# Kernel tuning notes

Measured on AMD Instinct MI355X. Metric: run time of the kernel, lower is better.

## Reference

```python
import jax, jax.numpy as jnp
import numpy as np

# Mamba2 hyperparameters (from init_kwargs + mamba_ssm defaults)
D_MODEL = 1024
D_STATE = 64
D_CONV = 4
EXPAND = 2
HEADDIM = 64                      # mamba_ssm default
D_INNER = EXPAND * D_MODEL        # 2048
NHEADS = D_INNER // HEADDIM       # 32
NGROUPS = 1
CONV_DIM = D_INNER + 2 * NGROUPS * D_STATE      # 2176
D_IN_PROJ = 2 * D_INNER + 2 * NGROUPS * D_STATE + NHEADS  # 4256
BATCH, SEQLEN = 4, 2048


def setup_inputs() -> dict:
    key = jax.random.key(0)
    ks = jax.random.split(key, 8)
    x = jax.random.normal(ks[0], (BATCH, SEQLEN, D_MODEL), dtype=jnp.float32)
    W_in = jax.random.normal(ks[1], (D_MODEL, D_IN_PROJ), dtype=jnp.float32) * 0.02
    conv_w = jax.random.normal(ks[2], (CONV_DIM, D_CONV), dtype=jnp.float32) * 0.2
    conv_b = jnp.zeros((CONV_DIM,), dtype=jnp.float32)
    # dt_bias = inverse-softplus of dt ~ U(1e-3, 0.1), as in mamba_ssm init
    dt = jnp.exp(jax.random.uniform(ks[3], (NHEADS,)) * (np.log(0.1) - np.log(1e-3)) + np.log(1e-3))
    dt_bias = dt + jnp.log(-jnp.expm1(-dt))
    A_log = jnp.log(jax.random.uniform(ks[4], (NHEADS,), minval=1.0, maxval=16.0))
    D = jnp.ones((NHEADS,), dtype=jnp.float32)
    norm_w = jnp.ones((D_INNER,), dtype=jnp.float32)
    W_out = jax.random.normal(ks[5], (D_INNER, D_MODEL), dtype=jnp.float32) * 0.02
    return {"x": x, "W_in": W_in, "conv_w": conv_w, "conv_b": conv_b,
            "dt_bias": dt_bias, "A_log": A_log, "D": D, "norm_w": norm_w, "W_out": W_out}


def _mamba2_forward(x, W_in, conv_w, conv_b, dt_bias, A_log, D, norm_w, W_out):
    Bsz, L, _ = x.shape
    zxbcdt = x @ W_in                                   # [B, L, D_IN_PROJ]
    z = zxbcdt[..., :D_INNER]                           # gate
    xBC = zxbcdt[..., D_INNER:D_INNER + CONV_DIM]
    dt = zxbcdt[..., D_INNER + CONV_DIM:]               # [B, L, H]
    dt = jax.nn.softplus(dt + dt_bias)

    # causal depthwise conv1d over time, kernel width D_CONV
    xp = jnp.pad(xBC, ((0, 0), (D_CONV - 1, 0), (0, 0)))
    xc = sum(xp[:, k:k + L, :] * conv_w[:, k] for k in range(D_CONV))
    xBC = jax.nn.silu(xc + conv_b)

    xh = xBC[..., :D_INNER].reshape(Bsz, L, NHEADS, HEADDIM)   # [B,L,H,P]
    Bm = xBC[..., D_INNER:D_INNER + D_STATE]                   # [B,L,N] (ngroups=1)
    Cm = xBC[..., D_INNER + D_STATE:]                          # [B,L,N]
    A = -jnp.exp(A_log)                                        # [H]

    # selective SSM scan: h_t = h_{t-1}*exp(dt_t*A) + dt_t * x_t (outer) B_t ; y_t = C_t . h_t
    def step(h, inp):
        dt_t, x_t, B_t, C_t = inp                 # [B,H],[B,H,P],[B,N],[B,N]
        dA = jnp.exp(dt_t * A)                    # [B,H]
        h = h * dA[..., None, None] + (dt_t[..., None] * x_t)[..., None] * B_t[:, None, None, :]
        y_t = jnp.einsum('bhpn,bn->bhp', h, C_t)
        return h, y_t

    h0 = jnp.zeros((Bsz, NHEADS, HEADDIM, D_STATE), dtype=x.dtype)
    inputs = (jnp.moveaxis(dt, 1, 0), jnp.moveaxis(xh, 1, 0),
              jnp.moveaxis(Bm, 1, 0), jnp.moveaxis(Cm, 1, 0))
    _, ys = jax.lax.scan(step, h0, inputs)                     # [L,B,H,P]
    y = jnp.moveaxis(ys, 0, 1) + xh * D[None, None, :, None]   # skip term D*x
    y = y.reshape(Bsz, L, D_INNER)

    # gated RMSNorm: norm(y * silu(z)) * weight
    y = y * jax.nn.silu(z)
    y = y * jax.lax.rsqrt(jnp.mean(y * y, axis=-1, keepdims=True) + 1e-5) * norm_w
    return y @ W_out


def reference(x, W_in, conv_w, conv_b, dt_bias, A_log, D, norm_w, W_out):
    return _mamba2_forward(x, W_in, conv_w, conv_b, dt_bias, A_log, D, norm_w, W_out)
```

## Files before the change

kernel.cpp:

```cpp
#include <hip/hip_runtime.h>
#include <hip/hip_bf16.h>

#define B_SZ   4
#define SEQ    2048
#define DM     1024
#define DIN    2048
#define DST    64
#define NH     32
#define HD     64
#define DPROJ  4256
#define NPROJ  4224
#define MROWS  (B_SZ*SEQ)
#define QC     64
#define NC     (SEQ/QC)


typedef __attribute__((ext_vector_type(8))) __bf16 bf16x8;
typedef __attribute__((ext_vector_type(4))) __bf16 bf16x4;
typedef __attribute__((ext_vector_type(4))) float  floatx4;

__device__ __forceinline__ int swz(int row, int col) {
    return row * 64 + ((((col >> 3) ^ (row & 7)) << 3) | (col & 7));
}
__device__ __forceinline__ float bfbits2f(unsigned short u) {
    return __uint_as_float(((unsigned int)u) << 16);
}
__device__ __forceinline__ float silu_f(float v) { return v / (1.f + __expf(-v)); }

__global__ __launch_bounds__(256) void prep_cvt_kernel(const float* __restrict__ x,
                                                       const float* __restrict__ W_in,
                                                       const float* __restrict__ W_out,
                                                       const float* __restrict__ norm_w,
                                                       __bf16* __restrict__ xbf,
                                                       __bf16* __restrict__ WinT,
                                                       __bf16* __restrict__ WoutT,
                                                       float* __restrict__ dtraw) {
    __shared__ float smem[16 * 132 + 4096];
    const int bid = blockIdx.x, tid = threadIdx.x;
    if (bid < 1568) {
        float (*tile)[129] = (float (*)[129])smem;
        const float* src; __bf16* dst; const float* scal; int Ksrc, Csrc, mb, kb;
        if (bid < 1056) {
            mb = bid >> 5; kb = bid & 31;
            src = W_in; dst = WinT; scal = nullptr; Ksrc = DM; Csrc = DPROJ;
        } else {
            int t = bid - 1056; mb = t >> 6; kb = t & 63;
            src = W_out; dst = WoutT; scal = norm_w; Ksrc = DIN; Csrc = DM;
        }
        const int K32 = Ksrc >> 5;
        #pragma unroll
        for (int i = 0; i < 4; i++) {
            int idx = tid + 256 * i;
            int kl = idx >> 5, c4 = idx & 31;
            int n = mb * 128 + c4 * 4;
            float4 v = make_float4(0.f, 0.f, 0.f, 0.f);
            if (n < Csrc) v = *(const float4*)(src + (size_t)(kb * 32 + kl) * Csrc + n);
            if (scal) { float s = scal[kb * 32 + kl]; v.x *= s; v.y *= s; v.z *= s; v.w *= s; }
            tile[kl][c4 * 4 + 0] = v.x; tile[kl][c4 * 4 + 1] = v.y;
            tile[kl][c4 * 4 + 2] = v.z; tile[kl][c4 * 4 + 3] = v.w;
        }
        __syncthreads();
        #pragma unroll
        for (int i = 0; i < 2; i++) {
            int c = tid + 256 * i;
            int sub = c >> 6, ln = c & 63, q = ln >> 4, lmn = ln & 15;
            bf16x8 o;
            #pragma unroll
            for (int e = 0; e < 8; e++) o[e] = (__bf16)tile[q * 8 + e][sub * 16 + lmn];
            *(bf16x8*)(dst + ((((size_t)(mb * 8 + sub)) * K32 + kb) << 9) + (ln << 3)) = o;
        }
        return;
    }
    float (*xs)[132] = (float (*)[132])smem;
    float* dtw = smem + 16 * 132;
    const int slabi = bid - 1568;
    const int r0 = slabi * 16;
    const int lm = tid & 15, pos = tid >> 4;
    const int rr = tid >> 4, h2 = (tid & 15) * 2;
    __bf16* slab = xbf + (size_t)slabi * (16 * DM);

    float a0 = 0.f, a1 = 0.f;
    for (int kc = 0; kc < 8; kc++) {
        #pragma unroll
        for (int i = 0; i < 2; i++) {
            int idx = tid + 256 * i;
            int row = idx >> 5, c4 = idx & 31;
            float4 v = ((const float4*)(x + (size_t)(r0 + row) * DM + kc * 128))[c4];
            xs[row][c4 * 4 + 0] = v.x; xs[row][c4 * 4 + 1] = v.y;
            xs[row][c4 * 4 + 2] = v.z; xs[row][c4 * 4 + 3] = v.w;
        }
        #pragma unroll
        for (int i = 0; i < 16; i++) {
            int idx = tid + 256 * i;
            dtw[idx] = W_in[(size_t)(kc * 128 + (idx >> 5)) * DPROJ + NPROJ + (idx & 31)];
        }
        __syncthreads();
        {
            bf16x8 o;
            #pragma unroll
            for (int e = 0; e < 8; e++) o[e] = (__bf16)xs[lm][pos * 8 + e];
            int kb = kc * 4 + (pos >> 2), q = pos & 3;
            *(bf16x8*)(slab + (size_t)(kb * 64 + q * 16 + lm) * 8) = o;
        }
        for (int j = 0; j < 128; j++) {
            float xv = xs[rr][j];
            a0 = fmaf(xv, dtw[j * 32 + h2], a0);
            a1 = fmaf(xv, dtw[j * 32 + h2 + 1], a1);
        }
        __syncthreads();
    }
    dtraw[(size_t)(r0 + rr) * NH + h2]     = a0;
    dtraw[(size_t)(r0 + rr) * NH + h2 + 1] = a1;
}

template<int STORE_BF16>
__device__ __forceinline__ void gemm_body(const __bf16* __restrict__ A,
                                          const __bf16* __restrict__ Bt,
                                          float* __restrict__ Cf,
                                          __bf16* __restrict__ Cb,
                                          const float* __restrict__ rowscale,
                                          int N, int K, int mb, int nb) {
    __shared__ __align__(16) __bf16 As[4096];
    __shared__ __align__(16) __bf16 Bs[4096];
    const int tid = threadIdx.x;
    const int wave = tid >> 6, lane = tid & 63;
    const int lm = lane & 15, lq = lane >> 4;
    const int K32 = K >> 5;

    floatx4 acc[4][4] = {};

    for (int kb = 0; kb < K32; kb++) {
        #pragma unroll
        for (int r = 0; r < 2; r++) {
            int c = tid + (r << 8);
            int sub = c >> 6, ln = c & 63;
            __builtin_amdgcn_global_load_lds(
                reinterpret_cast<const unsigned int*>(
                    A + ((((size_t)(mb * 8 + sub)) * K32 + kb) << 9) + (ln << 3)),
                reinterpret_cast<unsigned int*>(As + (size_t)c * 8), 16, 0, 0);
            __builtin_amdgcn_global_load_lds(
                reinterpret_cast<const unsigned int*>(
                    Bt + ((((size_t)(nb * 8 + sub)) * K32 + kb) << 9) + (ln << 3)),
                reinterpret_cast<unsigned int*>(Bs + (size_t)c * 8), 16, 0, 0);
        }
        __syncthreads();
        bf16x8 af[4], bfr[4];
        #pragma unroll
        for (int i = 0; i < 4; i++)
            af[i] = *(const bf16x8*)(As + ((((wave & 1) << 2) + i) << 9) + (lane << 3));
        #pragma unroll
        for (int i = 0; i < 4; i++)
            bfr[i] = *(const bf16x8*)(Bs + ((((wave >> 1) << 2) + i) << 9) + (lane << 3));
        #pragma unroll
        for (int mi = 0; mi < 4; mi++)
            #pragma unroll
            for (int ni = 0; ni < 4; ni++)
                acc[mi][ni] = __builtin_amdgcn_mfma_f32_16x16x32_bf16(af[mi], bfr[ni], acc[mi][ni], 0, 0, 0);
        __syncthreads();
    }

    const int wm = (wave & 1) << 6, wn = (wave >> 1) << 6;
    #pragma unroll
    for (int mi = 0; mi < 4; mi++) {
        #pragma unroll
        for (int r = 0; r < 4; r++) {
            int row = mb * 128 + wm + mi * 16 + lq * 4 + r;
            float s = 1.f;
            if (rowscale) s = rsqrtf(rowscale[row] * (1.f / (float)DIN) + 1e-5f);
            #pragma unroll
            for (int ni = 0; ni < 4; ni++) {
                int col = nb * 128 + wn + ni * 16 + lm;
                if (col < N) {
                    if (STORE_BF16) Cb[(size_t)row * N + col] = (__bf16)acc[mi][ni][r];
                    else            Cf[(size_t)row * N + col] = acc[mi][ni][r] * s;
                }
            }
        }
    }
}

__global__ __launch_bounds__(256) void gemm1_kernel(const __bf16* __restrict__ A,
                                                    const __bf16* __restrict__ Bt,
                                                    __bf16* __restrict__ Cb,
                                                    const float* __restrict__ dtraw,
                                                    const float* __restrict__ dt_bias,
                                                    const float* __restrict__ A_log,
                                                    float* __restrict__ dtv,
                                                    float* __restrict__ cum,
                                                    float* __restrict__ rowsum) {
    const int bid = blockIdx.x, tid = threadIdx.x;
    if (bid < 2112) {
        gemm_body<1>(A, Bt, nullptr, Cb, nullptr, NPROJ, DM, bid & 63, bid >> 6);
    } else if (bid < 2240) {
        const int blk = bid - 2112;
        const int b = blk >> 5, h = blk & 31;
        const int wave = tid >> 6, lane = tid & 63;
        float Ah = -__expf(A_log[h]);
        float dtb = dt_bias[h];
        for (int c = wave; c < NC; c += 4) {
            int t = c * QC + lane;
            float u = dtraw[((size_t)b * SEQ + t) * NH + h] + dtb;
            float d = fmaxf(u, 0.f) + log1pf(__expf(-fabsf(u)));
            float s = d * Ah;
            #pragma unroll
            for (int o = 1; o < 64; o <<= 1) {
                float v = __shfl_up(s, o);
                if (lane >= o) s += v;
            }
            size_t idx = (size_t)blk * SEQ + t;
            dtv[idx] = d;
            cum[idx] = s;
        }
    } else {
        float4 z = make_float4(0.f, 0.f, 0.f, 0.f);
        *(float4*)(rowsum + (size_t)(bid - 2240) * 1024 + tid * 4) = z;
    }
}

__global__ __launch_bounds__(256) void gemm2_kernel(const __bf16* __restrict__ A,
                                                    const __bf16* __restrict__ Bt,
                                                    float* __restrict__ Cf,
                                                    const float* __restrict__ rowscale) {
    gemm_body<0>(A, Bt, Cf, nullptr, rowscale, DM, DIN, blockIdx.x, blockIdx.y);
}

__global__ __launch_bounds__(256) void chunk_state_kernel(const __bf16* __restrict__ zx,
                                                          const float* __restrict__ cw,
                                                          const float* __restrict__ cb,
                                                          const float* __restrict__ dtv,
                                                          const float* __restrict__ cum,
                                                          __bf16* __restrict__ Sbuf) {
    const int blk = blockIdx.x;
    const int hq = blk & 7;
    const int bc = blk >> 3;
    const int c = bc & (NC - 1), b = bc >> 5;
    const int tid = threadIdx.x;
    const int wave = tid >> 6, lane = tid & 63;
    const int lm = lane & 15, q = lane >> 4;
    const int h = hq * 4 + wave;

    __shared__ __align__(16) __bf16 sBt[4096];
    __shared__ __align__(16) __bf16 sXw[4][4096];

    const __bf16* zb = zx + (size_t)b * SEQ * NPROJ;
    {
        const int rg = tid >> 5, cs = tid & 31;
        const int n0 = 2 * cs;
        float4 wA = *(const float4*)(cw + (size_t)(2048 + n0) * 4);
        float  bA = cb[2048 + n0];
        float4 wB = *(const float4*)(cw + (size_t)(2048 + n0 + 1) * 4);
        float  bB = cb[2048 + n0 + 1];
        unsigned int rv[11];
        const int tbase = c * QC + rg * 8 - 3;
        #pragma unroll
        for (int i = 0; i < 11; i++) {
            int t = tbase + i;
            rv[i] = (t >= 0) ? *(const unsigned int*)(zb + (size_t)t * NPROJ + 4096 + n0) : 0u;
        }
        bf16x8 olo, ohi;
        #pragma unroll
        for (int sl = 0; sl < 8; sl++) {
            float xl[4], xh[4];
            #pragma unroll
            for (int k = 0; k < 4; k++) {
                unsigned int u = rv[sl + k];
                xl[k] = bfbits2f((unsigned short)(u & 0xffff));
                xh[k] = bfbits2f((unsigned short)(u >> 16));
            }
            olo[sl] = (__bf16)silu_f(bA + wA.x*xl[0] + wA.y*xl[1] + wA.z*xl[2] + wA.w*xl[3]);
            ohi[sl] = (__bf16)silu_f(bB + wB.x*xh[0] + wB.y*xh[1] + wB.z*xh[2] + wB.w*xh[3]);
        }
        *(bf16x8*)&sBt[swz(n0,     rg * 8)] = olo;
        *(bf16x8*)&sBt[swz(n0 + 1, rg * 8)] = ohi;
    }
    const float* cump = cum + (size_t)(b * NH + h) * SEQ + (size_t)c * QC;
    const float* dtp  = dtv + (size_t)(b * NH + h) * SEQ + (size_t)c * QC;
    {
        const int cg = lane >> 3, rg = lane & 7;
        const int jx = h * 64 + cg * 8;
        float w4[8][4], bs[8];
        #pragma unroll
        for (int e = 0; e < 8; e++) {
            float4 w = *(const float4*)(cw + (size_t)(jx + e) * 4);
            w4[e][0] = w.x; w4[e][1] = w.y; w4[e][2] = w.z; w4[e][3] = w.w;
            bs[e] = cb[jx + e];
        }
        float rf[11][8];
        const int tbase = c * QC + rg * 8 - 3;
        #pragma unroll
        for (int i = 0; i < 11; i++) {
            int t = tbase + i;
            if (t >= 0) {
                bf16x8 v = *(const bf16x8*)(zb + (size_t)t * NPROJ + 2048 + jx);
                #pragma unroll
                for (int e = 0; e < 8; e++) rf[i][e] = (float)v[e];
            } else {
                #pragma unroll
                for (int e = 0; e < 8; e++) rf[i][e] = 0.f;
            }
        }
        float clast = cump[63];
        float wdt[8];
        #pragma unroll
        for (int sl = 0; sl < 8; sl++) {
            int s = rg * 8 + sl;
            wdt[sl] = dtp[s] * __expf(clast - cump[s]);
        }
        #pragma unroll
        for (int e = 0; e < 8; e++) {
            bf16x8 o;
            #pragma unroll
            for (int sl = 0; sl < 8; sl++) {
                float v = bs[e] + w4[e][0]*rf[sl][e] + w4[e][1]*rf[sl+1][e]
                                + w4[e][2]*rf[sl+2][e] + w4[e][3]*rf[sl+3][e];
                o[sl] = (__bf16)(silu_f(v) * wdt[sl]);
            }
            *(bf16x8*)&sXw[wave][swz(cg * 8 + e, rg * 8)] = o;
        }
    }
    __syncthreads();

    floatx4 acc[4][4] = {};
    #pragma unroll
    for (int kb = 0; kb < 2; kb++) {
        bf16x8 aX[4], bB[4];
        #pragma unroll
        for (int pi = 0; pi < 4; pi++)
            aX[pi] = *(const bf16x8*)(&sXw[wave][swz(pi * 16 + lm, kb * 32 + q * 8)]);
        #pragma unroll
        for (int ni = 0; ni < 4; ni++)
            bB[ni] = *(const bf16x8*)(&sBt[swz(ni * 16 + lm, kb * 32 + q * 8)]);
        #pragma unroll
        for (int pi = 0; pi < 4; pi++)
            #pragma unroll
            for (int ni = 0; ni < 4; ni++)
                acc[pi][ni] = __builtin_amdgcn_mfma_f32_16x16x32_bf16(aX[pi], bB[ni], acc[pi][ni], 0, 0, 0);
    }
    __bf16* Sp = Sbuf + ((size_t)(b * NC + c) * NH + h) * (HD * DST);
    #pragma unroll
    for (int pi = 0; pi < 4; pi++)
        #pragma unroll
        for (int r = 0; r < 4; r++) {
            int p = pi * 16 + q * 4 + r;
            #pragma unroll
            for (int ni = 0; ni < 4; ni++)
                Sp[p * 64 + ni * 16 + lm] = (__bf16)acc[pi][ni][r];
        }
}

__global__ __launch_bounds__(256) void state_scan_kernel(__bf16* __restrict__ Sbuf,
                                                         const float* __restrict__ cum) {
    int blk = blockIdx.x >> 2;
    int part = blockIdx.x & 3;
    int b = blk >> 5, h = blk & 31;
    int off = part * 1024 + threadIdx.x * 4;
    float run[4];
    #pragma unroll
    for (int n = 0; n < 4; n++) run[n] = 0.f;
    for (int c = 0; c < NC; c++) {
        __bf16* Sp = Sbuf + ((size_t)(b * NC + c) * NH + h) * (HD * DST) + off;
        bf16x4 sv = *(const bf16x4*)Sp;
        float tmp[4];
        #pragma unroll
        for (int n = 0; n < 4; n++) tmp[n] = (float)sv[n];
        bf16x4 ov;
        #pragma unroll
        for (int n = 0; n < 4; n++) ov[n] = (__bf16)run[n];
        *(bf16x4*)Sp = ov;
        float P = __expf(cum[(size_t)blk * SEQ + c * QC + QC - 1]);
        #pragma unroll
        for (int n = 0; n < 4; n++) run[n] = fmaf(run[n], P, tmp[n]);
    }
}

__global__ __launch_bounds__(128) void chunk_out_kernel(const __bf16* __restrict__ zx,
                                                        const float* __restrict__ cw,
                                                        const float* __restrict__ cb,
                                                        const float* __restrict__ dtv,
                                                        const float* __restrict__ cum,
                                                        const __bf16* __restrict__ Sbuf,
                                                        const float* __restrict__ Dv,
                                                        float* __restrict__ rowsum,
                                                        __bf16* __restrict__ y) {
    const int blk = blockIdx.x;
    const int hp = blk & 15;
    const int bc = blk >> 4;
    const int c = bc & (NC - 1), b = bc >> 5;
    const int tid = threadIdx.x;
    const int wave = tid >> 6, lane = tid & 63;
    const int lm = lane & 15, q = lane >> 4;
    const int h = hp * 2 + wave;

    __shared__ __align__(16) __bf16 smem[16384];
    __bf16* sB  = smem;
    __bf16* sC  = smem + 4096;
    __bf16* sXt = smem + 8192 + (wave << 12);
    __bf16* sP  = smem + (wave << 12);

    const __bf16* zb = zx + (size_t)b * SEQ * NPROJ;
    const size_t rowbase = (size_t)b * SEQ + (size_t)c * QC;
    {
        const int cg = lane >> 3, rg = lane & 7;
        const int jx = 2048 + wave * 64 + cg * 8;
        __bf16* sDst = wave ? sC : sB;
        float w4[8][4], bs[8];
        #pragma unroll
        for (int e = 0; e < 8; e++) {
            float4 w = *(const float4*)(cw + (size_t)(jx + e) * 4);
            w4[e][0] = w.x; w4[e][1] = w.y; w4[e][2] = w.z; w4[e][3] = w.w;
            bs[e] = cb[jx + e];
        }
        float rf[11][8];
        const int tbase = c * QC + rg * 8 - 3;
        #pragma unroll
        for (int i = 0; i < 11; i++) {
            int t = tbase + i;
            if (t >= 0) {
                bf16x8 v = *(const bf16x8*)(zb + (size_t)t * NPROJ + 2048 + jx);
                #pragma unroll
                for (int e = 0; e < 8; e++) rf[i][e] = (float)v[e];
            } else {
                #pragma unroll
                for (int e = 0; e < 8; e++) rf[i][e] = 0.f;
            }
        }
        #pragma unroll
        for (int sl = 0; sl < 8; sl++) {
            bf16x8 o;
            #pragma unroll
            for (int e = 0; e < 8; e++) {
                float v = bs[e] + w4[e][0]*rf[sl][e] + w4[e][1]*rf[sl+1][e]
                                + w4[e][2]*rf[sl+2][e] + w4[e][3]*rf[sl+3][e];
                o[e] = (__bf16)silu_f(v);
            }
            *(bf16x8*)&sDst[swz(rg * 8 + sl, cg * 8)] = o;
        }
    }
    {
        const int cg = lane >> 3, rg = lane & 7;
        const int jx = h * 64 + cg * 8;
        float w4[8][4], bs[8];
        #pragma unroll
        for (int e = 0; e < 8; e++) {
            float4 w = *(const float4*)(cw + (size_t)(jx + e) * 4);
            w4[e][0] = w.x; w4[e][1] = w.y; w4[e][2] = w.z; w4[e][3] = w.w;
            bs[e] = cb[jx + e];
        }
        float rf[11][8];
        const int tbase = c * QC + rg * 8 - 3;
        #pragma unroll
        for (int i = 0; i < 11; i++) {
            int t = tbase + i;
            if (t >= 0) {
                bf16x8 v = *(const bf16x8*)(zb + (size_t)t * NPROJ + 2048 + jx);
                #pragma unroll
                for (int e = 0; e < 8; e++) rf[i][e] = (float)v[e];
            } else {
                #pragma unroll
                for (int e = 0; e < 8; e++) rf[i][e] = 0.f;
            }
        }
        #pragma unroll
        for (int e = 0; e < 8; e++) {
            bf16x8 o;
            #pragma unroll
            for (int sl = 0; sl < 8; sl++) {
                float v = bs[e] + w4[e][0]*rf[sl][e] + w4[e][1]*rf[sl+1][e]
                                + w4[e][2]*rf[sl+2][e] + w4[e][3]*rf[sl+3][e];
                o[sl] = (__bf16)silu_f(v);
            }
            *(bf16x8*)&sXt[swz(cg * 8 + e, rg * 8)] = o;
        }
    }
    __syncthreads();

    const float* cump = cum + (size_t)(b * NH + h) * SEQ + (size_t)c * QC;
    const float* dtp  = dtv + (size_t)(b * NH + h) * SEQ + (size_t)c * QC;
    float cumv = cump[lane], dtvv = dtp[lane];
    float ct[4][4];
    #pragma unroll
    for (int ti = 0; ti < 4; ti++)
        #pragma unroll
        for (int r = 0; r < 4; r++)
            ct[ti][r] = __shfl(cumv, ti * 16 + q * 4 + r);
    float cums_l[4], dtv_l[4];
    #pragma unroll
    for (int si = 0; si < 4; si++) {
        cums_l[si] = __shfl(cumv, si * 16 + lm);
        dtv_l[si]  = __shfl(dtvv, si * 16 + lm);
    }

    bf16x8 afC[4][2];
    #pragma unroll
    for (int ti = 0; ti < 4; ti++)
        #pragma unroll
        for (int kb = 0; kb < 2; kb++)
            afC[ti][kb] = *(const bf16x8*)(&sC[swz(ti * 16 + lm, kb * 32 + q * 8)]);

    floatx4 accG[4][4] = {};
    #pragma unroll
    for (int kb = 0; kb < 2; kb++) {
        bf16x8 bfB[4];
        #pragma unroll
        for (int si = 0; si < 4; si++)
            bfB[si] = *(const bf16x8*)(&sB[swz(si * 16 + lm, kb * 32 + q * 8)]);
        #pragma unroll
        for (int ti = 0; ti < 4; ti++)
            #pragma unroll
            for (int si = 0; si < 4; si++)
                if (si <= ti)
                    accG[ti][si] = __builtin_amdgcn_mfma_f32_16x16x32_bf16(afC[ti][kb], bfB[si], accG[ti][si], 0, 0, 0);
    }
    __syncthreads();

    float Dh = Dv[h];
    #pragma unroll
    for (int ti = 0; ti < 4; ti++)
        #pragma unroll
        for (int si = 0; si < 4; si++) {
            if (si > ti) continue;
            #pragma unroll
            for (int r = 0; r < 4; r++) {
                int t = ti * 16 + q * 4 + r;
                float arg = fminf(ct[ti][r] - cums_l[si], 0.f);
                float val = dtv_l[si] * __expf(arg) * accG[ti][si][r];
                if (ti == si) {
                    if (lm > q * 4 + r) val = 0.f;
                    else if (lm == q * 4 + r) val += Dh;
                }
                sP[swz(t, si * 16 + lm)] = (__bf16)val;
            }
        }
    #pragma unroll
    for (int r = 0; r < 4; r++) {
        sP[swz(q * 4 + r, 16 + lm)] = (__bf16)0.f;
        sP[swz(32 + q * 4 + r, 48 + lm)] = (__bf16)0.f;
    }
    __syncthreads();

    floatx4 accY[4][4] = {};
    const __bf16* Sp = Sbuf + ((size_t)(b * NC + c) * NH + h) * (HD * DST);
    #pragma unroll
    for (int kb = 0; kb < 2; kb++) {
        bf16x8 bS[4];
        #pragma unroll
        for (int pi = 0; pi < 4; pi++)
            bS[pi] = *(const bf16x8*)(Sp + (pi * 16 + lm) * 64 + kb * 32 + q * 8);
        #pragma unroll
        for (int ti = 0; ti < 4; ti++)
            #pragma unroll
            for (int pi = 0; pi < 4; pi++)
                accY[ti][pi] = __builtin_amdgcn_mfma_f32_16x16x32_bf16(afC[ti][kb], bS[pi], accY[ti][pi], 0, 0, 0);
    }
    #pragma unroll
    for (int ti = 0; ti < 4; ti++)
        #pragma unroll
        for (int r = 0; r < 4; r++) {
            float e = __expf(ct[ti][r]);
            #pragma unroll
            for (int pi = 0; pi < 4; pi++)
                accY[ti][pi][r] *= e;
        }

    #pragma unroll
    for (int kb = 0; kb < 2; kb++) {
        bf16x8 bX[4];
        #pragma unroll
        for (int pi = 0; pi < 4; pi++)
            bX[pi] = *(const bf16x8*)(&sXt[swz(pi * 16 + lm, kb * 32 + q * 8)]);
        #pragma unroll
        for (int ti = 0; ti < 4; ti++) {
            if (ti < 2 * kb) continue;
            bf16x8 aP = *(const bf16x8*)(&sP[swz(ti * 16 + lm, kb * 32 + q * 8)]);
            #pragma unroll
            for (int pi = 0; pi < 4; pi++)
                accY[ti][pi] = __builtin_amdgcn_mfma_f32_16x16x32_bf16(aP, bX[pi], accY[ti][pi], 0, 0, 0);
        }
    }

    const int R4v = (int)(rowbase >> 4);
    #pragma unroll
    for (int ti = 0; ti < 4; ti++) {
        __bf16* slab = y + (size_t)(R4v + ti) * 32768;
        #pragma unroll
        for (int r = 0; r < 4; r++) {
            int t = ti * 16 + q * 4 + r;
            const __bf16* zrow = zx + (rowbase + t) * NPROJ + h * 64;
            float rs = 0.f;
            #pragma unroll
            for (int pi = 0; pi < 4; pi++) {
                float zv = (float)zrow[pi * 16 + lm];
                float g = accY[ti][pi][r] * silu_f(zv);
                rs += g * g;
                int kbC = h * 2 + (pi >> 1);
                int qC  = ((pi & 1) << 1) + (lm >> 3);
                slab[kbC * 512 + qC * 128 + (lm & 7) + (q * 4 + r) * 8] = (__bf16)g;
            }
            rs += __shfl_xor(rs, 1);
            rs += __shfl_xor(rs, 2);
            rs += __shfl_xor(rs, 4);
            rs += __shfl_xor(rs, 8);
            if (lm == 0) atomicAdd(&rowsum[rowbase + t], rs);
        }
    }
}

extern "C" void kernel_launch(void* const* d_in, const int* in_sizes, int n_in,
                              void* d_out, int out_size, void* d_ws, size_t ws_size,
                              hipStream_t stream) {
    const float* x       = (const float*)d_in[0];
    const float* W_in    = (const float*)d_in[1];
    const float* conv_w  = (const float*)d_in[2];
    const float* conv_b  = (const float*)d_in[3];
    const float* dt_bias = (const float*)d_in[4];
    const float* A_log   = (const float*)d_in[5];
    const float* Dv      = (const float*)d_in[6];
    const float* norm_w  = (const float*)d_in[7];
    const float* W_out   = (const float*)d_in[8];
    float* out = (float*)d_out;

    char* ws = (char*)d_ws;
    size_t off = 0;
    auto take = [&](size_t bytes) { void* p = ws + off; off = (off + bytes + 255) & ~(size_t)255; return p; };
    __bf16* xbf    = (__bf16*)take((size_t)MROWS * DM * 2);
    __bf16* WinT   = (__bf16*)take((size_t)NPROJ * DM * 2);
    __bf16* WoutT  = (__bf16*)take((size_t)DM * DIN * 2);
    __bf16* zx     = (__bf16*)take((size_t)MROWS * NPROJ * 2);
    __bf16* yf     = (__bf16*)take((size_t)MROWS * DIN * 2);
    float*  dtraw  = (float*) take((size_t)MROWS * NH * 4);
    float*  dtv    = (float*) take((size_t)B_SZ * NH * SEQ * 4);
    float*  cum    = (float*) take((size_t)B_SZ * NH * SEQ * 4);
    __bf16* Sbuf   = (__bf16*)take((size_t)B_SZ * NC * NH * HD * DST * 2);
    float*  rowsum = (float*) take((size_t)MROWS * 4);
    (void)ws_size;

    prep_cvt_kernel<<<dim3(2080), 256, 0, stream>>>(x, W_in, W_out, norm_w,
                                                    xbf, WinT, WoutT, dtraw);
    gemm1_kernel<<<dim3(2248), 256, 0, stream>>>(xbf, WinT, zx,
                                                 dtraw, dt_bias, A_log, dtv, cum, rowsum);
    chunk_state_kernel<<<dim3(B_SZ * NC * (NH / 4)), 256, 0, stream>>>(
        zx, conv_w, conv_b, dtv, cum, Sbuf);
    state_scan_kernel<<<dim3(B_SZ * NH * 4), 256, 0, stream>>>(Sbuf, cum);
    chunk_out_kernel<<<dim3(B_SZ * NC * (NH / 2)), 128, 0, stream>>>(
        zx, conv_w, conv_b, dtv, cum, Sbuf, Dv, rowsum, yf);
    gemm2_kernel<<<dim3(MROWS / 128, DM / 128), 256, 0, stream>>>(yf, WoutT, out, rowsum);
}
```

Baseline: 390.1 us.

## Split prep kernel into weight conversion and per-row x conversion with dt projection

The combined prep kernel is split into two launches. A weight kernel converts W_in and W_out to bf16 and also copies the dt columns of W_in into a compact buffer. A second kernel converts x to bf16 and computes the dt projection, with each block handling 4 rows and splitting K across 8 partial sums that are then reduced in shared memory. The old 16-row slab loop reloaded the strided dt weights for every slab and ran a long serial per-thread reduction. The new layout aims for more parallelism and coalesced weight reads, at the cost of one more launch and an extra buffer.

```diff
diff --git a/kernel.cpp b/kernel.cpp
--- a/kernel.cpp
+++ b/kernel.cpp
@@ -25,92 +25,105 @@
 __device__ __forceinline__ float bfbits2f(unsigned short u) {
     return __uint_as_float(((unsigned int)u) << 16);
 }
+__device__ __forceinline__ unsigned short f2bfbits(float f) {
+    union { __bf16 h; unsigned short u; } cv; cv.h = (__bf16)f; return cv.u;
+}
 __device__ __forceinline__ float silu_f(float v) { return v / (1.f + __expf(-v)); }
 
-__global__ __launch_bounds__(256) void prep_cvt_kernel(const float* __restrict__ x,
-                                                       const float* __restrict__ W_in,
-                                                       const float* __restrict__ W_out,
-                                                       const float* __restrict__ norm_w,
-                                                       __bf16* __restrict__ xbf,
-                                                       __bf16* __restrict__ WinT,
-                                                       __bf16* __restrict__ WoutT,
-                                                       float* __restrict__ dtraw) {
-    __shared__ float smem[16 * 132 + 4096];
+__global__ __launch_bounds__(256) void prep_weights_kernel(const float* __restrict__ W_in,
+                                                           const float* __restrict__ W_out,
+                                                           const float* __restrict__ norm_w,
+                                                           float* __restrict__ dtWc,
+                                                           __bf16* __restrict__ WinT,
+                                                           __bf16* __restrict__ WoutT) {
+    __shared__ float tile[32][129];
     const int bid = blockIdx.x, tid = threadIdx.x;
-    if (bid < 1568) {
-        float (*tile)[129] = (float (*)[129])smem;
-        const float* src; __bf16* dst; const float* scal; int Ksrc, Csrc, mb, kb;
-        if (bid < 1056) {
-            mb = bid >> 5; kb = bid & 31;
-            src = W_in; dst = WinT; scal = nullptr; Ksrc = DM; Csrc = DPROJ;
-        } else {
-            int t = bid - 1056; mb = t >> 6; kb = t & 63;
-            src = W_out; dst = WoutT; scal = norm_w; Ksrc = DIN; Csrc = DM;
-        }
-        const int K32 = Ksrc >> 5;
-        #pragma unroll
-        for (int i = 0; i < 4; i++) {
-            int idx = tid + 256 * i;
-            int kl = idx >> 5, c4 = idx & 31;
-            int n = mb * 128 + c4 * 4;
-            float4 v = make_float4(0.f, 0.f, 0.f, 0.f);
-            if (n < Csrc) v = *(const float4*)(src + (size_t)(kb * 32 + kl) * Csrc + n);
-            if (scal) { float s = scal[kb * 32 + kl]; v.x *= s; v.y *= s; v.z *= s; v.w *= s; }
-            tile[kl][c4 * 4 + 0] = v.x; tile[kl][c4 * 4 + 1] = v.y;
-            tile[kl][c4 * 4 + 2] = v.z; tile[kl][c4 * 4 + 3] = v.w;
-        }
-        __syncthreads();
-        #pragma unroll
-        for (int i = 0; i < 2; i++) {
-            int c = tid + 256 * i;
-            int sub = c >> 6, ln = c & 63, q = ln >> 4, lmn = ln & 15;
-            bf16x8 o;
-            #pragma unroll
-            for (int e = 0; e < 8; e++) o[e] = (__bf16)tile[q * 8 + e][sub * 16 + lmn];
-            *(bf16x8*)(dst + ((((size_t)(mb * 8 + sub)) * K32 + kb) << 9) + (ln << 3)) = o;
-        }
+    if (bid < 128) {
+        int idx = bid * 256 + tid;
+        int k = idx >> 5, h = idx & 31;
+        dtWc[idx] = W_in[(size_t)k * DPROJ + NPROJ + h];
         return;
     }
-    float (*xs)[132] = (float (*)[132])smem;
-    float* dtw = smem + 16 * 132;
-    const int slabi = bid - 1568;
-    const int r0 = slabi * 16;
-    const int lm = tid & 15, pos = tid >> 4;
-    const int rr = tid >> 4, h2 = (tid & 15) * 2;
-    __bf16* slab = xbf + (size_t)slabi * (16 * DM);
-
-    float a0 = 0.f, a1 = 0.f;
-    for (int kc = 0; kc < 8; kc++) {
-        #pragma unroll
-        for (int i = 0; i < 2; i++) {
-            int idx = tid + 256 * i;
-            int row = idx >> 5, c4 = idx & 31;
-            float4 v = ((const float4*)(x + (size_t)(r0 + row) * DM + kc * 128))[c4];
-            xs[row][c4 * 4 + 0] = v.x; xs[row][c4 * 4 + 1] = v.y;
-            xs[row][c4 * 4 + 2] = v.z; xs[row][c4 * 4 + 3] = v.w;
-        }
-        #pragma unroll
-        for (int i = 0; i < 16; i++) {
-            int idx = tid + 256 * i;
-            dtw[idx] = W_in[(size_t)(kc * 128 + (idx >> 5)) * DPROJ + NPROJ + (idx & 31)];
-        }
-        __syncthreads();
-        {
-            bf16x8 o;
-            #pragma unroll
-            for (int e = 0; e < 8; e++) o[e] = (__bf16)xs[lm][pos * 8 + e];
-            int kb = kc * 4 + (pos >> 2), q = pos & 3;
-            *(bf16x8*)(slab + (size_t)(kb * 64 + q * 16 + lm) * 8) = o;
-        }
-        for (int j = 0; j < 128; j++) {
-            float xv = xs[rr][j];
-            a0 = fmaf(xv, dtw[j * 32 + h2], a0);
-            a1 = fmaf(xv, dtw[j * 32 + h2 + 1], a1);
-        }
-        __syncthreads();
-    }
-    dtraw[(size_t)(r0 + rr) * NH + h2]     = a0;
-    dtraw[(size_t)(r0 + rr) * NH + h2 + 1] = a1;
+    const float* src; __bf16* dst; const float* scal; int Ksrc, Csrc, mb, kb;
+    if (bid < 128 + 1056) {
+        int t = bid - 128; mb = t >> 5; kb = t & 31;
+        src = W_in; dst = WinT; scal = nullptr; Ksrc = DM; Csrc = DPROJ;
+    } else {
+        int t = bid - 1184; mb = t >> 6; kb = t & 63;
+        src = W_out; dst = WoutT; scal = norm_w; Ksrc = DIN; Csrc = DM;
+    }
+    const int K32 = Ksrc >> 5;
+    #pragma unroll
+    for (int i = 0; i < 4; i++) {
+        int idx = tid + 256 * i;
+        int kl = idx >> 5, c4 = idx & 31;
+        int n = mb * 128 + c4 * 4;
+        float4 v = make_float4(0.f, 0.f, 0.f, 0.f);
+        if (n < Csrc) v = *(const float4*)(src + (size_t)(kb * 32 + kl) * Csrc + n);
+        if (scal) { float s = scal[kb * 32 + kl]; v.x *= s; v.y *= s; v.z *= s; v.w *= s; }
+        tile[kl][c4 * 4 + 0] = v.x; tile[kl][c4 * 4 + 1] = v.y;
+        tile[kl][c4 * 4 + 2] = v.z; tile[kl][c4 * 4 + 3] = v.w;
+    }
+    __syncthreads();
+    #pragma unroll
+    for (int i = 0; i < 2; i++) {
+        int c = tid + 256 * i;
+        int sub = c >> 6, ln = c & 63, q = ln >> 4, lmn = ln & 15;
+        bf16x8 o;
+        #pragma unroll
+        for (int e = 0; e < 8; e++) o[e] = (__bf16)tile[q * 8 + e][sub * 16 + lmn];
+        *(bf16x8*)(dst + ((((size_t)(mb * 8 + sub)) * K32 + kb) << 9) + (ln << 3)) = o;
+    }
+}
+
+__global__ __launch_bounds__(256) void cvt_dt_kernel(const float* __restrict__ x,
+                                                     const float* __restrict__ dtWc,
+                                                     __bf16* __restrict__ xbf,
+                                                     float* __restrict__ dtraw) {
+    __shared__ float xs[4][DM];
+    __shared__ float red[4][8][32];
+    const int row0 = blockIdx.x * 4;
+    const int tid = threadIdx.x;
+    #pragma unroll
+    for (int r = 0; r < 4; r++) {
+        float4 v = ((const float4*)(x + (size_t)(row0 + r) * DM))[tid];
+        xs[r][tid * 4 + 0] = v.x; xs[r][tid * 4 + 1] = v.y;
+        xs[r][tid * 4 + 2] = v.z; xs[r][tid * 4 + 3] = v.w;
+    }
+    __syncthreads();
+    __bf16* slab = xbf + (size_t)(row0 >> 4) * (16 * DM);
+    const int lmb = row0 & 15;
+    #pragma unroll
+    for (int i = 0; i < 2; i++) {
+        int g = tid + 256 * i;
+        int r = g >> 7, pos = g & 127;
+        int kb = pos >> 2, q = pos & 3;
+        bf16x8 o;
+        #pragma unroll
+        for (int e = 0; e < 8; e++) o[e] = (__bf16)xs[r][pos * 8 + e];
+        *(bf16x8*)(slab + (size_t)(kb * 64 + q * 16 + lmb + r) * 8) = o;
+    }
+    const int part = tid >> 5, h = tid & 31;
+    const float* wb = dtWc + part * 128 * 32 + h;
+    const int kb0 = part * 128;
+    float s0 = 0.f, s1 = 0.f, s2 = 0.f, s3 = 0.f;
+    for (int j = 0; j < 128; j++) {
+        float w = wb[j * 32];
+        s0 = fmaf(xs[0][kb0 + j], w, s0);
+        s1 = fmaf(xs[1][kb0 + j], w, s1);
+        s2 = fmaf(xs[2][kb0 + j], w, s2);
+        s3 = fmaf(xs[3][kb0 + j], w, s3);
+    }
+    red[0][part][h] = s0; red[1][part][h] = s1;
+    red[2][part][h] = s2; red[3][part][h] = s3;
+    __syncthreads();
+    if (tid < 128) {
+        int r = tid >> 5, hh = tid & 31;
+        float s = 0.f;
+        #pragma unroll
+        for (int p = 0; p < 8; p++) s += red[r][p][hh];
+        dtraw[(size_t)(row0 + r) * NH + hh] = s;
+    }
 }
 
 template<int STORE_BF16>
@@ -631,11 +644,12 @@
     float*  dtv    = (float*) take((size_t)B_SZ * NH * SEQ * 4);
     float*  cum    = (float*) take((size_t)B_SZ * NH * SEQ * 4);
     __bf16* Sbuf   = (__bf16*)take((size_t)B_SZ * NC * NH * HD * DST * 2);
+    float*  dtWc   = (float*) take((size_t)DM * NH * 4);
     float*  rowsum = (float*) take((size_t)MROWS * 4);
     (void)ws_size;
 
-    prep_cvt_kernel<<<dim3(2080), 256, 0, stream>>>(x, W_in, W_out, norm_w,
-                                                    xbf, WinT, WoutT, dtraw);
+    prep_weights_kernel<<<dim3(1696), 256, 0, stream>>>(W_in, W_out, norm_w, dtWc, WinT, WoutT);
+    cvt_dt_kernel<<<dim3(MROWS / 4), 256, 0, stream>>>(x, dtWc, xbf, dtraw);
     gemm1_kernel<<<dim3(2248), 256, 0, stream>>>(xbf, WinT, zx,
                                                  dtraw, dt_bias, A_log, dtv, cum, rowsum);
     chunk_state_kernel<<<dim3(B_SZ * NC * (NH / 4)), 256, 0, stream>>>(
```

Measured after the change: 360.3 us. -7.6%, faster.
